# Kernel tuning notes

Measured on AMD Instinct MI355X. Metric: run time of the kernel, lower is better.

## Reference

```python
import jax, jax.numpy as jnp
import numpy as np

VOCAB = 32000
EMBED = 512
NUM_CLASS = 5
LEAVES = 8192
N_NODES = 2 * LEAVES - 1


def _build_tree(n_leaves):
    """Balanced binary tree over n_leaves leaves, nodes listed in post-order
    (children always appear before their parent), matching the recursive
    traversal order of the original torch module."""
    is_leaf, word, left, right = [], [], [], []

    def rec(lo, hi):
        if hi - lo == 1:
            is_leaf.append(1)
            word.append((lo * 2654435761) % VOCAB)
            left.append(0)
            right.append(0)
        else:
            mid = (lo + hi) // 2
            l = rec(lo, mid)
            r = rec(mid, hi)
            is_leaf.append(0)
            word.append(0)
            left.append(l)
            right.append(r)
        return len(is_leaf) - 1

    rec(0, n_leaves)
    return (np.asarray(is_leaf, np.int32), np.asarray(word, np.int32),
            np.asarray(left, np.int32), np.asarray(right, np.int32))


def setup_inputs() -> dict:
    key = jax.random.key(0)
    k1, k2, k3, k4, k5 = jax.random.split(key, 5)
    is_leaf, word, left, right = _build_tree(LEAVES)
    scale = 0.05
    return {
        "is_leaf": jnp.asarray(is_leaf),
        "word": jnp.asarray(word),
        "left": jnp.asarray(left),
        "right": jnp.asarray(right),
        "emb": jax.random.normal(k1, (VOCAB, EMBED), jnp.float32) * scale,
        "W": jax.random.normal(k2, (EMBED, 2 * EMBED), jnp.float32) * scale,
        "bW": jax.random.normal(k3, (EMBED,), jnp.float32) * scale,
        "P": jax.random.normal(k4, (NUM_CLASS, EMBED), jnp.float32) * scale,
        "bP": jax.random.normal(k5, (NUM_CLASS,), jnp.float32) * scale,
    }


def reference(is_leaf, word, left, right, emb, W, bW, P, bP):
    n = is_leaf.shape[0]

    def step(H, xs):
        idx, lf, wd, li, ri = xs
        # internal node: relu(W @ [h_left; h_right] + b)
        pair = jnp.concatenate([H[li], H[ri]])          # [2D]
        internal = pair @ W.T + bW                       # [D]
        leaf = emb[wd]                                   # [D]
        h = jax.nn.relu(jnp.where(lf == 1, leaf, internal))
        return H.at[idx].set(h), None

    H0 = jnp.zeros((n, EMBED), emb.dtype)
    xs = (jnp.arange(n, dtype=jnp.int32), is_leaf, word, left, right)
    H, _ = jax.lax.scan(step, H0, xs)
    # per-node class logits, rows in traversal (post-)order: [N, num_class]
    return H @ P.T + bP
```

## Files before the change

### kernel.cpp

```cpp
#include <hip/hip_runtime.h>


#define EMBED 512
#define K2    1024
#define WOFF  (EMBED * K2)

typedef _Float16 half8 __attribute__((ext_vector_type(8)));
typedef float    floatx4 __attribute__((ext_vector_type(4)));

__device__ __forceinline__ float relu_f(float x) { return fmaxf(x, 0.0f); }

#define GLDS16(gp, lp)                                                        \
    __builtin_amdgcn_global_load_lds(                                         \
        (const __attribute__((address_space(1))) void*)(gp),                  \
        (__attribute__((address_space(3))) void*)(lp), 16, 0, 0)

#define MFMA16(a, b, c) __builtin_amdgcn_mfma_f32_16x16x32_f16(a, b, c, 0, 0, 0)

__global__ __launch_bounds__(256)
void packleaf(const float* __restrict__ W, const float* __restrict__ emb,
              const int* __restrict__ word,
              _Float16* __restrict__ Whp,
              _Float16* __restrict__ Hh, _Float16* __restrict__ Hl,
              int nLeaves)
{
    int tid = threadIdx.x;
    int wave = tid >> 6, lane = tid & 63;

    {
        int t = blockIdx.x * 256 + tid;
        int n = t >> 7, kc = t & 127;
        const float* src = W + (size_t)n * K2 + kc * 8;
        int s = kc >> 2, quad = kc & 3;
        int ln = (quad << 4) | (n & 15);
        size_t off = (size_t)(n >> 4) * 16384 + (size_t)s * 512 + (size_t)ln * 8;
        half8 hi, lo;
#pragma unroll
        for (int j = 0; j < 8; ++j) {
            float w = src[j];
            _Float16 h16 = (_Float16)w;
            hi[j] = h16;
            lo[j] = (_Float16)(w - (float)h16);
        }
        *(half8*)(Whp + off) = hi;
        *(half8*)(Whp + WOFF + off) = lo;
    }
    {
#pragma unroll
        for (int i = 0; i < 8; ++i) {
            int m = blockIdx.x * 32 + wave * 8 + i;
            if (m < nLeaves) {
                int wd = word[2 * m - __popc(m)];
                const float4* src = (const float4*)(emb + (size_t)wd * EMBED) + lane * 2;
                float4 a = src[0], b = src[1];
                float v[8] = {a.x, a.y, a.z, a.w, b.x, b.y, b.z, b.w};
                half8 hi, lo;
#pragma unroll
                for (int j = 0; j < 8; ++j) {
                    float x = relu_f(v[j]);
                    _Float16 h16 = (_Float16)x;
                    hi[j] = h16;
                    lo[j] = (_Float16)(x - (float)h16);
                }
                *(half8*)(Hh + (size_t)m * EMBED + lane * 8) = hi;
                *(half8*)(Hl + (size_t)m * EMBED + lane * 8) = lo;
            }
        }
    }
}

template <int BNF>
__global__ __launch_bounds__(256, 2)
void gemm_big(const _Float16* __restrict__ Ap,
              const _Float16* __restrict__ Wp,
              const float* __restrict__ bW,
              _Float16* __restrict__ Cp,
              int hoff)
{
    __shared__ _Float16 As[32768];

    int tid = threadIdx.x;
    int w = tid >> 6, lane = tid & 63;
    int q = lane >> 4, r = lane & 15;
    int bm0 = blockIdx.x * 128;
    int bn0 = blockIdx.y * (BNF * 16);

    const _Float16* Asrc = Ap + (size_t)(bm0 + w * 32 + r) * 1024 + q * 8;

    floatx4 acc[2][BNF];
#pragma unroll
    for (int t2 = 0; t2 < 2; ++t2)
#pragma unroll
        for (int u = 0; u < BNF; ++u) acc[t2][u] = (floatx4){0.f, 0.f, 0.f, 0.f};

#pragma unroll
    for (int t2 = 0; t2 < 2; ++t2)
#pragma unroll
        for (int s2 = 0; s2 < 2; ++s2)
#pragma unroll
            for (int hl = 0; hl < 2; ++hl) {
                const _Float16* gp = Asrc + (size_t)hl * hoff
                                   + t2 * (16 * 1024) + s2 * 32;
                GLDS16(gp, &As[(((w * 2 + t2) * 2 + s2) * 2 + hl) * 512]);
            }

    for (int kc = 0; kc < 16; ++kc) {
        int buf = kc & 1;
        if (kc < 15) {
#pragma unroll
            for (int t2 = 0; t2 < 2; ++t2)
#pragma unroll
                for (int s2 = 0; s2 < 2; ++s2)
#pragma unroll
                    for (int hl = 0; hl < 2; ++hl) {
                        const _Float16* gp = Asrc + (size_t)hl * hoff
                                           + t2 * (16 * 1024) + (kc + 1) * 64 + s2 * 32;
                        GLDS16(gp, &As[((buf ^ 1) * 32
                                        + ((w * 2 + t2) * 2 + s2) * 2 + hl) * 512]);
                    }
            asm volatile("s_waitcnt vmcnt(8)" ::: "memory");
        } else {
            asm volatile("s_waitcnt vmcnt(0)" ::: "memory");
        }

#pragma unroll
        for (int s2 = 0; s2 < 2; ++s2) {
            half8 ah[2], al[2];
#pragma unroll
            for (int t2 = 0; t2 < 2; ++t2) {
                int slot = buf * 32 + ((w * 2 + t2) * 2 + s2) * 2;
                ah[t2] = *(const half8*)&As[slot * 512 + lane * 8];
                al[t2] = *(const half8*)&As[(slot + 1) * 512 + lane * 8];
            }
#pragma unroll
            for (int u = 0; u < BNF; ++u) {
                const _Float16* pb = Wp + (size_t)(blockIdx.y * BNF + u) * 16384
                                   + (size_t)(kc * 2 + s2) * 512 + lane * 8;
                half8 bh = *(const half8*)pb;
                half8 bl = *(const half8*)(pb + WOFF);
#pragma unroll
                for (int t2 = 0; t2 < 2; ++t2) {
                    acc[t2][u] = MFMA16(ah[t2], bh, acc[t2][u]);
                    acc[t2][u] = MFMA16(ah[t2], bl, acc[t2][u]);
                    acc[t2][u] = MFMA16(al[t2], bh, acc[t2][u]);
                }
            }
        }
    }

#pragma unroll
    for (int t2 = 0; t2 < 2; ++t2)
#pragma unroll
        for (int u = 0; u < BNF; ++u) {
            int col = bn0 + u * 16 + r;
            float bw = bW[col];
#pragma unroll
            for (int reg = 0; reg < 4; ++reg) {
                int row = bm0 + (w * 2 + t2) * 16 + q * 4 + reg;
                float x = relu_f(acc[t2][u][reg] + bw);
                _Float16 hi = (_Float16)x;
                size_t o = (size_t)row * EMBED + col;
                Cp[o] = hi;
                Cp[o + hoff] = (_Float16)(x - (float)hi);
            }
        }
}

__global__ __launch_bounds__(256)
void gemm_splitk32(const _Float16* __restrict__ Ap, const _Float16* __restrict__ Wp,
                   const float* __restrict__ bW,
                   _Float16* __restrict__ Cp, int hoff)
{
    __shared__ float red[4096];

    int tid = threadIdx.x;
    int wave = tid >> 6, lane = tid & 63;
    int q = lane >> 4, r = lane & 15;
    int m0 = blockIdx.x * 32, n0 = blockIdx.y * 32;

    const _Float16 *pAh[2], *pAl[2];
#pragma unroll
    for (int mi = 0; mi < 2; ++mi) {
        int m = m0 + mi * 16 + r;
        int prow = 2 * m + (wave >> 1);
        int kb = (wave & 1) * 256;
        pAh[mi] = Ap + (size_t)prow * EMBED + kb + q * 8;
        pAl[mi] = pAh[mi] + hoff;
    }
    const _Float16* pB[2];
#pragma unroll
    for (int u = 0; u < 2; ++u)
        pB[u] = Wp + (size_t)(blockIdx.y * 2 + u) * 16384
              + (size_t)(wave * 8) * 512 + lane * 8;

    floatx4 acc[2][2];
#pragma unroll
    for (int mi = 0; mi < 2; ++mi)
#pragma unroll
        for (int u = 0; u < 2; ++u) acc[mi][u] = (floatx4){0.f, 0.f, 0.f, 0.f};

#pragma unroll
    for (int s = 0; s < 8; ++s) {
        half8 ah[2], al[2], bh[2], bl[2];
#pragma unroll
        for (int mi = 0; mi < 2; ++mi) {
            ah[mi] = *(const half8*)(pAh[mi] + s * 32);
            al[mi] = *(const half8*)(pAl[mi] + s * 32);
        }
#pragma unroll
        for (int u = 0; u < 2; ++u) {
            bh[u] = *(const half8*)(pB[u] + s * 512);
            bl[u] = *(const half8*)(pB[u] + s * 512 + WOFF);
        }
#pragma unroll
        for (int mi = 0; mi < 2; ++mi)
#pragma unroll
            for (int u = 0; u < 2; ++u) {
                acc[mi][u] = MFMA16(ah[mi], bh[u], acc[mi][u]);
                acc[mi][u] = MFMA16(ah[mi], bl[u], acc[mi][u]);
                acc[mi][u] = MFMA16(al[mi], bh[u], acc[mi][u]);
            }
    }

#pragma unroll
    for (int mi = 0; mi < 2; ++mi)
#pragma unroll
        for (int u = 0; u < 2; ++u)
#pragma unroll
            for (int reg = 0; reg < 4; ++reg)
                red[wave * 1024 + (mi * 16 + q * 4 + reg) * 32 + u * 16 + r]
                    = acc[mi][u][reg];
    __syncthreads();

    int row = tid >> 3, c4 = (tid & 7) * 4;
    _Float16 hi4[4], lo4[4];
#pragma unroll
    for (int j = 0; j < 4; ++j) {
        int c = row * 32 + c4 + j;
        float v = red[c] + red[1024 + c] + red[2048 + c] + red[3072 + c];
        float x = relu_f(v + bW[n0 + c4 + j]);
        _Float16 hi = (_Float16)x;
        hi4[j] = hi;
        lo4[j] = (_Float16)(x - (float)hi);
    }
    size_t o = (size_t)(m0 + row) * EMBED + n0 + c4;
#pragma unroll
    for (int j = 0; j < 4; ++j) { Cp[o + j] = hi4[j]; Cp[o + hoff + j] = lo4[j]; }
}

__global__ __launch_bounds__(256)
void gemm_splitk(const _Float16* __restrict__ Ap, const _Float16* __restrict__ Wp,
                 const float* __restrict__ bW,
                 _Float16* __restrict__ Cp, int hoff, int M)
{
    __shared__ float red[1024];

    int tid = threadIdx.x;
    int wave = tid >> 6, lane = tid & 63;
    int q = lane >> 4, r = lane & 15;
    int mt = blockIdx.x, u = blockIdx.y;

    int m = mt * 16 + r;
    if (m >= M) m = M - 1;
    int prow = 2 * m + (wave >> 1);
    int kb = (wave & 1) * 256;
    const _Float16* pAh = Ap + (size_t)prow * EMBED + kb + q * 8;
    const _Float16* pAl = pAh + hoff;
    const _Float16* pB  = Wp + (size_t)u * 16384 + (size_t)(wave * 8) * 512 + lane * 8;

    floatx4 acc = (floatx4){0.f, 0.f, 0.f, 0.f};
#pragma unroll
    for (int s = 0; s < 8; ++s) {
        half8 ah = *(const half8*)(pAh + s * 32);
        half8 al = *(const half8*)(pAl + s * 32);
        half8 bh = *(const half8*)(pB + s * 512);
        half8 bl = *(const half8*)(pB + s * 512 + WOFF);
        acc = MFMA16(ah, bh, acc);
        acc = MFMA16(ah, bl, acc);
        acc = MFMA16(al, bh, acc);
    }
#pragma unroll
    for (int reg = 0; reg < 4; ++reg)
        red[wave * 256 + (q * 4 + reg) * 16 + r] = acc[reg];
    __syncthreads();

    int row = tid >> 4, col = tid & 15;
    float v = red[row * 16 + col] + red[256 + row * 16 + col]
            + red[512 + row * 16 + col] + red[768 + row * 16 + col];
    int mm = mt * 16 + row;
    if (mm < M) {
        int colg = u * 16 + col;
        float x = relu_f(v + bW[colg]);
        _Float16 hi = (_Float16)x;
        size_t o = (size_t)mm * EMBED + colg;
        Cp[o] = hi;
        Cp[o + hoff] = (_Float16)(x - (float)hi);
    }
}

__global__ __launch_bounds__(256)
void out_kernel(const _Float16* __restrict__ Hh, const _Float16* __restrict__ Hl,
                const float* __restrict__ P, const float* __restrict__ bP,
                float* __restrict__ out, int nNodes)
{
    int t = blockIdx.x * 256 + threadIdx.x;
    int j = t >> 6, lane = t & 63;
    if (j >= nNodes) return;
    int v = nNodes - j;
    int h = 13 - (31 - __clz(v));
    int m = j - ((nNodes + 1) - (1 << (13 - h + 1)));
    int node = ((m + 1) << (h + 1)) - 2 - __popc(m);

    half8 hv = *(const half8*)(Hh + (size_t)j * EMBED + lane * 8);
    half8 lv = *(const half8*)(Hl + (size_t)j * EMBED + lane * 8);
    float hx[8];
#pragma unroll
    for (int k = 0; k < 8; ++k) hx[k] = (float)hv[k] + (float)lv[k];
    float s[5];
#pragma unroll
    for (int c = 0; c < 5; ++c) {
        const float* p = P + c * EMBED + lane * 8;
        float4 p0 = *(const float4*)p;
        float4 p1 = *(const float4*)(p + 4);
        s[c] = hx[0] * p0.x + hx[1] * p0.y + hx[2] * p0.z + hx[3] * p0.w
             + hx[4] * p1.x + hx[5] * p1.y + hx[6] * p1.z + hx[7] * p1.w;
    }
#pragma unroll
    for (int o = 32; o > 0; o >>= 1)
#pragma unroll
        for (int c = 0; c < 5; ++c)
            s[c] += __shfl_down(s[c], o, 64);
    if (lane == 0) {
#pragma unroll
        for (int c = 0; c < 5; ++c)
            out[(size_t)node * 5 + c] = s[c] + bP[c];
    }
}

extern "C" void kernel_launch(void* const* d_in, const int* in_sizes, int n_in,
                              void* d_out, int out_size, void* d_ws, size_t ws_size,
                              hipStream_t stream)
{
    const int*   word = (const int*)d_in[1];
    const float* emb  = (const float*)d_in[4];
    const float* W    = (const float*)d_in[5];
    const float* bW   = (const float*)d_in[6];
    const float* P    = (const float*)d_in[7];
    const float* bP   = (const float*)d_in[8];
    float* out = (float*)d_out;

    int nNodes  = in_sizes[0];
    int nLeaves = (nNodes + 1) / 2;
    int nRows   = nNodes + 1;

    int hoff = nRows * EMBED;
    _Float16* Hh  = (_Float16*)d_ws;
    _Float16* Hl  = Hh + hoff;
    _Float16* Whp = Hl + hoff;

    auto roff = [&](int h) { return nRows - (1 << (14 - h)); };

    packleaf<<<dim3(256), dim3(256), 0, stream>>>(
        W, emb, word, Whp, Hh, Hl, nLeaves);

    gemm_big<8><<<dim3(32, 4), dim3(256), 0, stream>>>(
        Hh + (size_t)roff(0) * EMBED, Whp, bW,
        Hh + (size_t)roff(1) * EMBED, hoff);
    gemm_big<4><<<dim3(16, 8), dim3(256), 0, stream>>>(
        Hh + (size_t)roff(1) * EMBED, Whp, bW,
        Hh + (size_t)roff(2) * EMBED, hoff);

    for (int h = 3; h <= 4; ++h) {
        int M = 1 << (13 - h);
        gemm_splitk32<<<dim3(M / 32, 16), dim3(256), 0, stream>>>(
            Hh + (size_t)roff(h - 1) * EMBED, Whp, bW,
            Hh + (size_t)roff(h) * EMBED, hoff);
    }
    for (int h = 5; h <= 13; ++h) {
        int M = 1 << (13 - h);
        gemm_splitk<<<dim3((M + 15) / 16, 32), dim3(256), 0, stream>>>(
            Hh + (size_t)roff(h - 1) * EMBED, Whp, bW,
            Hh + (size_t)roff(h) * EMBED, hoff, M);
    }
    out_kernel<<<dim3((nNodes * 64 + 255) / 256), dim3(256), 0, stream>>>(
        Hh, Hl, P, bP, out, nNodes);
}
```

Baseline: 290.3 us.

## Replace big GEMM with intra-block split-K over 8 waves and LDS reduction

Replaces the templated double-buffered gemm_big with a 512-thread kernel in which two wave groups each handle half of K and then combine their partial sums through shared memory. The first level now uses a 32x8 grid with 64-column tiles instead of 32x4, so more blocks and more waves are in flight for the two largest levels. The trade-off is that the asynchronous double-buffered prefetch is dropped in favour of a load followed by __syncthreads each K step, and an extra LDS reduction pass is added at the end.

```diff
diff --git a/kernel.cpp b/kernel.cpp
--- a/kernel.cpp
+++ b/kernel.cpp
@@ -69,73 +69,56 @@
     }
 }
 
-template <int BNF>
-__global__ __launch_bounds__(256, 2)
-void gemm_big(const _Float16* __restrict__ Ap,
-              const _Float16* __restrict__ Wp,
-              const float* __restrict__ bW,
-              _Float16* __restrict__ Cp,
-              int hoff)
+__global__ __launch_bounds__(512, 1)
+void gemm_lvl2(const _Float16* __restrict__ Ap,
+               const _Float16* __restrict__ Wp,
+               const float* __restrict__ bW,
+               _Float16* __restrict__ Cp,
+               int hoff)
 {
     __shared__ _Float16 As[32768];
+    __shared__ float Red[8192];
 
     int tid = threadIdx.x;
     int w = tid >> 6, lane = tid & 63;
     int q = lane >> 4, r = lane & 15;
-    int bm0 = blockIdx.x * 128;
-    int bn0 = blockIdx.y * (BNF * 16);
-
-    const _Float16* Asrc = Ap + (size_t)(bm0 + w * 32 + r) * 1024 + q * 8;
-
-    floatx4 acc[2][BNF];
+    int slice = w & 1, rowq = w >> 1;
+    int bm0 = blockIdx.x * 128, bn0 = blockIdx.y * 64;
+
+    floatx4 acc[2][4];
 #pragma unroll
     for (int t2 = 0; t2 < 2; ++t2)
 #pragma unroll
-        for (int u = 0; u < BNF; ++u) acc[t2][u] = (floatx4){0.f, 0.f, 0.f, 0.f};
-
-#pragma unroll
-    for (int t2 = 0; t2 < 2; ++t2)
-#pragma unroll
-        for (int s2 = 0; s2 < 2; ++s2)
-#pragma unroll
-            for (int hl = 0; hl < 2; ++hl) {
-                const _Float16* gp = Asrc + (size_t)hl * hoff
-                                   + t2 * (16 * 1024) + s2 * 32;
-                GLDS16(gp, &As[(((w * 2 + t2) * 2 + s2) * 2 + hl) * 512]);
-            }
-
-    for (int kc = 0; kc < 16; ++kc) {
-        int buf = kc & 1;
-        if (kc < 15) {
-#pragma unroll
-            for (int t2 = 0; t2 < 2; ++t2)
-#pragma unroll
-                for (int s2 = 0; s2 < 2; ++s2)
-#pragma unroll
-                    for (int hl = 0; hl < 2; ++hl) {
-                        const _Float16* gp = Asrc + (size_t)hl * hoff
-                                           + t2 * (16 * 1024) + (kc + 1) * 64 + s2 * 32;
-                        GLDS16(gp, &As[((buf ^ 1) * 32
-                                        + ((w * 2 + t2) * 2 + s2) * 2 + hl) * 512]);
-                    }
-            asm volatile("s_waitcnt vmcnt(8)" ::: "memory");
-        } else {
-            asm volatile("s_waitcnt vmcnt(0)" ::: "memory");
-        }
+        for (int u = 0; u < 4; ++u) acc[t2][u] = (floatx4){0.f, 0.f, 0.f, 0.f};
+
+    for (int kc = 0; kc < 8; ++kc) {
+#pragma unroll
+        for (int t2 = 0; t2 < 2; ++t2)
+#pragma unroll
+            for (int s2 = 0; s2 < 2; ++s2)
+#pragma unroll
+                for (int hl = 0; hl < 2; ++hl) {
+                    int rg = rowq * 2 + t2;
+                    const _Float16* gp = Ap + (size_t)(hl ? hoff : 0)
+                                       + (size_t)(bm0 + rg * 16 + r) * 1024
+                                       + slice * 512 + kc * 64 + s2 * 32 + q * 8;
+                    GLDS16(gp, &As[(((slice * 8 + rg) * 2 + s2) * 2 + hl) * 512]);
+                }
+        __syncthreads();
 
 #pragma unroll
         for (int s2 = 0; s2 < 2; ++s2) {
             half8 ah[2], al[2];
 #pragma unroll
             for (int t2 = 0; t2 < 2; ++t2) {
-                int slot = buf * 32 + ((w * 2 + t2) * 2 + s2) * 2;
-                ah[t2] = *(const half8*)&As[slot * 512 + lane * 8];
-                al[t2] = *(const half8*)&As[(slot + 1) * 512 + lane * 8];
-            }
-#pragma unroll
-            for (int u = 0; u < BNF; ++u) {
-                const _Float16* pb = Wp + (size_t)(blockIdx.y * BNF + u) * 16384
-                                   + (size_t)(kc * 2 + s2) * 512 + lane * 8;
+                int sb = ((slice * 8 + rowq * 2 + t2) * 2 + s2) * 2;
+                ah[t2] = *(const half8*)&As[sb * 512 + lane * 8];
+                al[t2] = *(const half8*)&As[(sb + 1) * 512 + lane * 8];
+            }
+#pragma unroll
+            for (int u = 0; u < 4; ++u) {
+                const _Float16* pb = Wp + (size_t)(blockIdx.y * 4 + u) * 16384
+                                   + (size_t)(slice * 16 + kc * 2 + s2) * 512 + lane * 8;
                 half8 bh = *(const half8*)pb;
                 half8 bl = *(const half8*)(pb + WOFF);
 #pragma unroll
@@ -146,24 +129,40 @@
                 }
             }
         }
-    }
-
-#pragma unroll
-    for (int t2 = 0; t2 < 2; ++t2)
-#pragma unroll
-        for (int u = 0; u < BNF; ++u) {
-            int col = bn0 + u * 16 + r;
-            float bw = bW[col];
-#pragma unroll
-            for (int reg = 0; reg < 4; ++reg) {
-                int row = bm0 + (w * 2 + t2) * 16 + q * 4 + reg;
-                float x = relu_f(acc[t2][u][reg] + bw);
-                _Float16 hi = (_Float16)x;
-                size_t o = (size_t)row * EMBED + col;
-                Cp[o] = hi;
-                Cp[o + hoff] = (_Float16)(x - (float)hi);
-            }
-        }
+        __syncthreads();
+    }
+
+    if (slice == 1) {
+#pragma unroll
+        for (int t2 = 0; t2 < 2; ++t2)
+#pragma unroll
+            for (int u = 0; u < 4; ++u)
+#pragma unroll
+                for (int reg = 0; reg < 4; ++reg)
+                    Red[(rowq * 32 + t2 * 16 + q * 4 + reg) * 64 + u * 16 + r]
+                        = acc[t2][u][reg];
+    }
+    __syncthreads();
+    if (slice == 0) {
+#pragma unroll
+        for (int t2 = 0; t2 < 2; ++t2)
+#pragma unroll
+            for (int u = 0; u < 4; ++u) {
+                int col = bn0 + u * 16 + r;
+                float bw = bW[col];
+#pragma unroll
+                for (int reg = 0; reg < 4; ++reg) {
+                    int ml = rowq * 32 + t2 * 16 + q * 4 + reg;
+                    float v = acc[t2][u][reg]
+                            + Red[ml * 64 + u * 16 + r];
+                    float x = relu_f(v + bw);
+                    _Float16 hi = (_Float16)x;
+                    size_t o = (size_t)(bm0 + ml) * EMBED + col;
+                    Cp[o] = hi;
+                    Cp[o + hoff] = (_Float16)(x - (float)hi);
+                }
+            }
+    }
 }
 
 __global__ __launch_bounds__(256)
@@ -363,10 +362,10 @@
     packleaf<<<dim3(256), dim3(256), 0, stream>>>(
         W, emb, word, Whp, Hh, Hl, nLeaves);
 
-    gemm_big<8><<<dim3(32, 4), dim3(256), 0, stream>>>(
+    gemm_lvl2<<<dim3(32, 8), dim3(512), 0, stream>>>(
         Hh + (size_t)roff(0) * EMBED, Whp, bW,
         Hh + (size_t)roff(1) * EMBED, hoff);
-    gemm_big<4><<<dim3(16, 8), dim3(256), 0, stream>>>(
+    gemm_lvl2<<<dim3(16, 8), dim3(512), 0, stream>>>(
         Hh + (size_t)roff(1) * EMBED, Whp, bW,
         Hh + (size_t)roff(2) * EMBED, hoff);
 
```

After: 256.7 us. 11.6% less time.
